# Kernel tuning notes

Hardware: AMD Instinct MI355X
Metric: run time of the kernel (lower is better)

The kernel has to match this reference:

```python
import jax, jax.numpy as jnp
import numpy as np

H, W = 480, 640  # config['loader']['resolution']
N = H * W
EPS = 1e-9


def _grid_indices():
    # matches torch.meshgrid(arange(H), arange(W)) stacked as (y, x): [1, N, 2]
    my, mx = jnp.meshgrid(jnp.arange(H, dtype=jnp.float32),
                          jnp.arange(W, dtype=jnp.float32), indexing='ij')
    return jnp.stack([my, mx], axis=-1).reshape(1, N, 2)


def setup_inputs() -> dict:
    key = jax.random.key(0)
    k1, k2 = jax.random.split(key)
    B, P = 8, 4
    return {
        'flow_maps_x': jax.random.normal(k1, (B, P, H, W), jnp.float32),
        'flow_maps_y': jax.random.normal(k2, (B, P, H, W), jnp.float32),
        'i': 0,
        'tref': 4,
    }


def reference(flow_maps_x, flow_maps_y, i, tref):
    B = flow_maps_x.shape[0]
    indices = _grid_indices()  # [1, N, 2] (y, x)

    # get_event_flow at the integer pixel grid == flattening the i-th flow map
    fy = flow_maps_y[:, i].reshape(B, N)
    fx = flow_maps_x[:, i].reshape(B, N)
    indices_flow = jnp.stack([fy, fx], axis=-1)  # [B, N, 2] (flow_y, flow_x)

    # event_propagation: warp grid to tref
    dt = jnp.asarray(tref - i, dtype=flow_maps_x.dtype)
    warped = indices + dt * indices_flow  # [B, N, 2]

    # purge_unfeasible: zero out mask for points leaving the image
    inside = ((warped[..., 0] >= 0) & (warped[..., 0] <= H - 1) &
              (warped[..., 1] >= 0) & (warped[..., 1] <= W - 1))
    mask = inside.astype(warped.dtype)[..., None]  # [B, N, 1]

    # get_interpolation: 4 bilinear neighbors, weights = prod of axis weights
    top_y = jnp.floor(warped[..., 0:1]); bot_y = top_y + 1.0
    left_x = jnp.floor(warped[..., 1:2]); right_x = left_x + 1.0
    idx = jnp.concatenate([
        jnp.concatenate([top_y, left_x], -1),
        jnp.concatenate([top_y, right_x], -1),
        jnp.concatenate([bot_y, left_x], -1),
        jnp.concatenate([bot_y, right_x], -1)], axis=1)  # [B, 4N, 2]
    ev4 = jnp.tile(warped, (1, 4, 1))
    w = jnp.clip(1.0 - jnp.abs(ev4 - idx), 0.0, 1.0)
    weights = w[..., 0:1] * w[..., 1:2]  # [B, 4N, 1]

    mask4 = jnp.tile(mask, (1, 4, 1))
    flow4 = jnp.tile(indices_flow, (1, 4, 1))
    flat = (idx[..., 0] * W + idx[..., 1]).astype(jnp.int32)  # [B, 4N]
    batch_ix = jnp.arange(B)[:, None]

    def splat(vals):  # vals [B, 4N, 1] -> [B, 1, H, W] scatter-add
        v = (vals * mask4)[..., 0]
        img = jnp.zeros((B, N), vals.dtype).at[batch_ix, flat].add(v, mode='drop')
        return img.reshape(B, 1, H, W)

    warped_weights = splat(weights)
    warped_flow_y = splat(weights * flow4[..., 0:1]) / (warped_weights + EPS)
    warped_flow_x = splat(weights * flow4[..., 1:2]) / (warped_weights + EPS)
    return warped_flow_x, warped_flow_y
```

## Files before the change

### kernel.cpp

```cpp
#include <hip/hip_runtime.h>
#include <stdint.h>

#define HH 480
#define WW 640
#define NN (HH * WW)
#define BB 8
#define PP 4
#define EPS 1e-9f

#define TW 64
#define TH 32
#define HALO 12
#define RGW (TW + 2 * HALO)
#define RGH (TH + 2 * HALO)
#define RGN (RGW * RGH)
#define NBX (WW / TW)
#define NBY (HH / TH)
#define NBLOCKS (NBX * NBY * BB)

#define BINSX (TW + 1)
#define BINSY (TH + 1)
#define NBINS (BINSX * BINSY)
#define CAP 4

#define SAFE_ID ((HALO << 7) | HALO)

#define SEGCAP 1024

__device__ __forceinline__ void gatomic(float* p, float v) {
    unsafeAtomicAdd(p, v);
}

__global__ __launch_bounds__(256)
void interleave_flow(const float* __restrict__ fx_all,
                     const float* __restrict__ fy_all,
                     const int* __restrict__ i_ptr,
                     float2* __restrict__ fxy2) {
    int t = blockIdx.x * blockDim.x + threadIdx.x;
    const int Q = NN / 4;
    if (t >= BB * Q) return;
    int b = t / Q, q = t - b * Q;
    int i = *i_ptr;
    const float4* fyp = (const float4*)(fy_all + (size_t)(b * PP + i) * NN);
    const float4* fxp = (const float4*)(fx_all + (size_t)(b * PP + i) * NN);
    float4 y4 = fyp[q], x4 = fxp[q];
    float2* o = fxy2 + (size_t)b * NN + (size_t)q * 4;
    o[0] = make_float2(y4.x, x4.x);
    o[1] = make_float2(y4.y, x4.y);
    o[2] = make_float2(y4.z, x4.z);
    o[3] = make_float2(y4.w, x4.w);
}

__global__ __launch_bounds__(256, 4)
void bin_gather_splat(const float2* __restrict__ fxy2,
                      const int* __restrict__ i_ptr,
                      const int* __restrict__ tref_ptr,
                      float* __restrict__ Sw, float* __restrict__ Swy, float* __restrict__ Swx,
                      unsigned* __restrict__ segcnt, int4* __restrict__ llist,
                      float* __restrict__ out) {
    __shared__ unsigned cnt[NBINS];
    __shared__ ushort4  ids4[NBINS];
    __shared__ unsigned lseg;
    const int tid = threadIdx.x;
    for (int e = tid; e < NBINS; e += 256) cnt[e] = 0;
    if (tid == 0) lseg = 0;
    __syncthreads();

    const int bx = blockIdx.x, by = blockIdx.y, b = blockIdx.z;
    const int bid = (b * NBY + by) * NBX + bx;
    int4* __restrict__ lseg_base = llist + (size_t)bid * SEGCAP;
    const int tx0 = bx * TW, ty0 = by * TH;
    const float dt = (float)(*tref_ptr - *i_ptr);
    const float2* __restrict__ fp2 = fxy2 + (size_t)b * NN;
    const size_t BN = (size_t)BB * NN;

    for (int sp = tid; sp < RGN; sp += 256) {
        int sy = sp / RGW, sx = sp - sy * RGW;
        int gy = ty0 - HALO + sy, gx = tx0 - HALO + sx;
        if ((unsigned)gy >= (unsigned)HH || (unsigned)gx >= (unsigned)WW) continue;
        int p = gy * WW + gx;
        float2 f2 = fp2[p];
        float fy = f2.x, fx = f2.y;
        float wyf = (float)gy + dt * fy;
        float wxf = (float)gx + dt * fx;
        if (!(wyf >= 0.0f && wyf <= (float)(HH - 1) &&
              wxf >= 0.0f && wxf <= (float)(WW - 1))) continue;
        float tyf = floorf(wyf), lxf = floorf(wxf);
        int iy0 = (int)tyf, ix0 = (int)lxf;
        int br = iy0 - ty0, bc = ix0 - tx0;

        bool overflow = false;
        if (br >= -1 && br < TH && bc >= -1 && bc < TW) {
            int bin = (br + 1) * BINSX + (bc + 1);
            unsigned slot = atomicAdd(&cnt[bin], 1u);
            if (slot < CAP)
                ((unsigned short*)&ids4[bin])[slot] = (unsigned short)((sy << 7) | sx);
            else overflow = true;
        }
        bool interior = ((unsigned)(gx - tx0) < (unsigned)TW) &&
                        ((unsigned)(gy - ty0) < (unsigned)TH);
        if (overflow || interior) {
            float fry = wyf - tyf, frx = wxf - lxf;
            float wts[4] = {(1.0f - fry) * (1.0f - frx),
                            (1.0f - fry) * frx,
                            fry * (1.0f - frx),
                            fry * frx};
#pragma unroll
            for (int k = 0; k < 4; ++k) {
                int iy = iy0 + (k >> 1), ix = ix0 + (k & 1);
                if ((unsigned)iy >= (unsigned)HH || (unsigned)ix >= (unsigned)WW) continue;
                bool inT = ((unsigned)(iy - ty0) < (unsigned)TH) &&
                           ((unsigned)(ix - tx0) < (unsigned)TW);
                int tnx = (ix >> 6) << 6;
                int tny = (iy >> 5) << 5;
                int ddx = gx < tnx ? tnx - gx : (gx > tnx + (TW - 1) ? gx - tnx - (TW - 1) : 0);
                int ddy = gy < tny ? tny - gy : (gy > tny + (TH - 1) ? gy - tny - (TH - 1) : 0);
                bool far = (ddx > HALO) || (ddy > HALO);
                if ((interior && far) || (overflow && inT)) {
                    int fi = b * NN + iy * WW + ix;
                    float w = wts[k];
                    unsigned slot = atomicAdd(&lseg, 1u);
                    if (slot < SEGCAP)
                        lseg_base[slot] = make_int4(fi, __float_as_int(w),
                                                    __float_as_int(w * fy),
                                                    __float_as_int(w * fx));
                }
            }
        }
    }
    __syncthreads();
    if (tid == 0) segcnt[bid] = lseg > SEGCAP ? SEGCAP : lseg;

    {
        const int c  = tid & 63;
        const int r0 = (tid >> 6) * 8;
        const float cxf = (float)(tx0 + c);

#define LOAD_SLOT(dst, idraw, nn, T) {                                        \
        bool valid = (unsigned)(T) < (nn);                                    \
        int sid = valid ? (int)(idraw) : SAFE_ID;                             \
        int sy_ = sid >> 7, sx_ = sid & 127;                                  \
        int gy_ = ty0 - HALO + sy_, gx_ = tx0 - HALO + sx_;                   \
        float2 f2_ = fp2[gy_ * WW + gx_];                                     \
        float wyf_ = (float)gy_ + dt * f2_.x;                                 \
        float wxf_ = (float)gx_ + dt * f2_.y;                                 \
        dst.x = valid ? wyf_ : -1.0e6f;                                       \
        dst.y = valid ? wxf_ : -1.0e6f;                                       \
        dst.z = f2_.x; dst.w = f2_.y; }

#define LOAD_ROW(d0,d1,d2,d3,d4,d5,d6,d7, brow) {                             \
        int bin0_ = (brow) * BINSX + c;                                       \
        unsigned na_ = cnt[bin0_];     ushort4 sa_ = ids4[bin0_];             \
        unsigned nb_ = cnt[bin0_ + 1]; ushort4 sb_ = ids4[bin0_ + 1];         \
        LOAD_SLOT(d0, sa_.x, na_, 0); LOAD_SLOT(d1, sa_.y, na_, 1);           \
        LOAD_SLOT(d2, sa_.z, na_, 2); LOAD_SLOT(d3, sa_.w, na_, 3);           \
        LOAD_SLOT(d4, sb_.x, nb_, 0); LOAD_SLOT(d5, sb_.y, nb_, 1);           \
        LOAD_SLOT(d6, sb_.z, nb_, 2); LOAD_SLOT(d7, sb_.w, nb_, 3); }

#define EVAL_SLOT(S) {                                                        \
        float ay_ = fmaxf(1.0f - fabsf(S.x - cyf), 0.0f);                     \
        float ax_ = fmaxf(1.0f - fabsf(S.y - cxf), 0.0f);                     \
        float w_ = ay_ * ax_;                                                 \
        ws += w_; wys += w_ * S.z; wxs += w_ * S.w; }

        float4 a0,a1,a2,a3,a4,a5,a6,a7;
        float4 b0,b1,b2,b3,b4,b5,b6,b7;
        LOAD_ROW(a0,a1,a2,a3,a4,a5,a6,a7, r0);
#pragma unroll
        for (int rr = 0; rr < 8; ++rr) {
            int r = r0 + rr;
            LOAD_ROW(b0,b1,b2,b3,b4,b5,b6,b7, r + 1);
            float cyf = (float)(ty0 + r);
            float ws = 0.f, wys = 0.f, wxs = 0.f;
            EVAL_SLOT(a0); EVAL_SLOT(a1); EVAL_SLOT(a2); EVAL_SLOT(a3);
            EVAL_SLOT(a4); EVAL_SLOT(a5); EVAL_SLOT(a6); EVAL_SLOT(a7);
            EVAL_SLOT(b0); EVAL_SLOT(b1); EVAL_SLOT(b2); EVAL_SLOT(b3);
            EVAL_SLOT(b4); EVAL_SLOT(b5); EVAL_SLOT(b6); EVAL_SLOT(b7);
            size_t o = (size_t)b * NN + (size_t)(ty0 + r) * WW + (tx0 + c);
            Sw[o] = ws; Swy[o] = wys; Swx[o] = wxs;
            float d = ws + EPS;
            out[o]      = wxs / d;
            out[BN + o] = wys / d;
            a0 = b0; a1 = b1; a2 = b2; a3 = b3;
            a4 = b4; a5 = b5; a6 = b6; a7 = b7;
        }
#undef LOAD_SLOT
#undef LOAD_ROW
#undef EVAL_SLOT
    }
}

__global__ __launch_bounds__(256)
void fix_add(const unsigned* __restrict__ segcnt, const int4* __restrict__ llist,
             float* __restrict__ Sw, float* __restrict__ Swy, float* __restrict__ Swx) {
    unsigned e = blockIdx.x * blockDim.x + threadIdx.x;
    unsigned seg = e / SEGCAP, idx = e - seg * SEGCAP;
    if (seg >= NBLOCKS || idx >= segcnt[seg]) return;
    int4 v = llist[e];
    gatomic(&Sw[v.x],  __int_as_float(v.y));
    gatomic(&Swy[v.x], __int_as_float(v.z));
    gatomic(&Swx[v.x], __int_as_float(v.w));
}

__global__ __launch_bounds__(256)
void fix_write(const unsigned* __restrict__ segcnt, const int4* __restrict__ llist,
               const float* __restrict__ Sw, const float* __restrict__ Swy,
               const float* __restrict__ Swx, float* __restrict__ out) {
    unsigned e = blockIdx.x * blockDim.x + threadIdx.x;
    unsigned seg = e / SEGCAP, idx = e - seg * SEGCAP;
    if (seg >= NBLOCKS || idx >= segcnt[seg]) return;
    int fi = llist[e].x;
    float d = Sw[fi] + EPS;
    out[fi] = Swx[fi] / d;
    out[(size_t)BB * NN + fi] = Swy[fi] / d;
}


__global__ void splat_kernel(const float* __restrict__ fx_all,
                             const float* __restrict__ fy_all,
                             const int* __restrict__ i_ptr,
                             const int* __restrict__ tref_ptr,
                             float* __restrict__ sum_w,
                             float* __restrict__ sum_wy,
                             float* __restrict__ sum_wx) {
    int t = blockIdx.x * blockDim.x + threadIdx.x;
    if (t >= BB * NN) return;
    int b = t / NN;
    int p = t - b * NN;
    int i = *i_ptr;
    float dt = (float)(*tref_ptr - i);
    const float fx = fx_all[(size_t)(b * PP + i) * NN + p];
    const float fy = fy_all[(size_t)(b * PP + i) * NN + p];
    float gy = (float)(p / WW);
    float gx = (float)(p - (p / WW) * WW);
    float wy = gy + dt * fy;
    float wx = gx + dt * fx;
    bool inside = (wy >= 0.0f) && (wy <= (float)(HH - 1)) &&
                  (wx >= 0.0f) && (wx <= (float)(WW - 1));
    if (!inside) return;
    float ty = floorf(wy);
    float lx = floorf(wx);
    int base = b * NN;
#pragma unroll
    for (int k = 0; k < 4; ++k) {
        float ny = ty + (float)(k >> 1);
        float nx = lx + (float)(k & 1);
        int iy = (int)ny;
        int ix = (int)nx;
        if (iy < 0 || iy >= HH || ix < 0 || ix >= WW) continue;
        float wgt_y = fminf(fmaxf(1.0f - fabsf(wy - ny), 0.0f), 1.0f);
        float wgt_x = fminf(fmaxf(1.0f - fabsf(wx - nx), 0.0f), 1.0f);
        float w = wgt_y * wgt_x;
        int fi = base + iy * WW + ix;
        gatomic(&sum_w[fi],  w);
        gatomic(&sum_wy[fi], w * fy);
        gatomic(&sum_wx[fi], w * fx);
    }
}

__global__ void finalize_kernel(const float* __restrict__ sum_w,
                                const float* __restrict__ sum_wy,
                                const float* __restrict__ sum_wx,
                                float* __restrict__ out) {
    int t = blockIdx.x * blockDim.x + threadIdx.x;
    if (t >= BB * NN) return;
    float denom = sum_w[t] + EPS;
    out[t]                   = sum_wx[t] / denom;
    out[(size_t)BB * NN + t] = sum_wy[t] / denom;
}


extern "C" void kernel_launch(void* const* d_in, const int* in_sizes, int n_in,
                              void* d_out, int out_size, void* d_ws, size_t ws_size,
                              hipStream_t stream) {
    const float* fx_all = (const float*)d_in[0];
    const float* fy_all = (const float*)d_in[1];
    const int* i_ptr    = (const int*)d_in[2];
    const int* tref_ptr = (const int*)d_in[3];
    float* out = (float*)d_out;

    const size_t BN = (size_t)BB * NN;
    const size_t s_bytes = 3 * BN * sizeof(float);
    const size_t f_bytes = BN * sizeof(float2);
    const size_t l_bytes = (size_t)NBLOCKS * SEGCAP * sizeof(int4);
    const size_t need = s_bytes + f_bytes + l_bytes + NBLOCKS * sizeof(unsigned);
    if (ws_size >= need) {
        float* Sw  = (float*)d_ws;
        float* Swy = Sw  + BN;
        float* Swx = Swy + BN;
        float2* fxy2 = (float2*)((char*)d_ws + s_bytes);
        int4* llist = (int4*)((char*)fxy2 + f_bytes);
        unsigned* segcnt = (unsigned*)((char*)llist + l_bytes);

        int itotal = (int)(BN / 4);
        interleave_flow<<<(itotal + 255) / 256, 256, 0, stream>>>(
            fx_all, fy_all, i_ptr, fxy2);
        dim3 grid(NBX, NBY, BB);
        bin_gather_splat<<<grid, 256, 0, stream>>>(fxy2, i_ptr, tref_ptr,
                                                   Sw, Swy, Swx, segcnt, llist, out);
        int fgrid = (NBLOCKS * SEGCAP) / 256;
        fix_add<<<fgrid, 256, 0, stream>>>(segcnt, llist, Sw, Swy, Swx);
        fix_write<<<fgrid, 256, 0, stream>>>(segcnt, llist, Sw, Swy, Swx, out);
    } else {
        float* sum_w  = (float*)d_ws;
        float* sum_wy = sum_w + BN;
        float* sum_wx = sum_wy + BN;
        hipMemsetAsync(d_ws, 0, 3 * BN * sizeof(float), stream);
        int total = (int)BN;
        int block = 256;
        int grid1 = (total + block - 1) / block;
        splat_kernel<<<grid1, block, 0, stream>>>(fx_all, fy_all, i_ptr, tref_ptr,
                                                  sum_w, sum_wy, sum_wx);
        finalize_kernel<<<grid1, block, 0, stream>>>(sum_w, sum_wy, sum_wx, out);
    }
}
```

Measured before the change: 71.73 us.

## Widen tiles to 128 columns and gather two output pixels per thread

Doubles the tile width so each block covers 128x32 pixels with the same 256 threads, and each thread now produces two adjacent output columns. The shared middle bin column is loaded once and evaluated for both pixels, and results are stored as float2. This reduces halo overhead per tile and redundant bin/flow gathers. In exchange it raises register pressure (occupancy hint lowered to 3), enlarges shared memory and the per-block overflow list, and packs source ids with 8-bit x fields.

Measured after the change: 89.28 us. +24.5%, slower.

```diff
diff --git a/kernel.cpp b/kernel.cpp
--- a/kernel.cpp
+++ b/kernel.cpp
@@ -8,7 +8,7 @@
 #define PP 4
 #define EPS 1e-9f
 
-#define TW 64
+#define TW 128
 #define TH 32
 #define HALO 12
 #define RGW (TW + 2 * HALO)
@@ -23,9 +23,9 @@
 #define NBINS (BINSX * BINSY)
 #define CAP 4
 
-#define SAFE_ID ((HALO << 7) | HALO)
-
-#define SEGCAP 1024
+#define SAFE_ID ((HALO << 8) | HALO)
+
+#define SEGCAP 2048
 
 __device__ __forceinline__ void gatomic(float* p, float v) {
     unsafeAtomicAdd(p, v);
@@ -51,7 +51,7 @@
     o[3] = make_float2(y4.w, x4.w);
 }
 
-__global__ __launch_bounds__(256, 4)
+__global__ __launch_bounds__(256, 3)
 void bin_gather_splat(const float2* __restrict__ fxy2,
                       const int* __restrict__ i_ptr,
                       const int* __restrict__ tref_ptr,
@@ -94,7 +94,7 @@
             int bin = (br + 1) * BINSX + (bc + 1);
             unsigned slot = atomicAdd(&cnt[bin], 1u);
             if (slot < CAP)
-                ((unsigned short*)&ids4[bin])[slot] = (unsigned short)((sy << 7) | sx);
+                ((unsigned short*)&ids4[bin])[slot] = (unsigned short)((sy << 8) | sx);
             else overflow = true;
         }
         bool interior = ((unsigned)(gx - tx0) < (unsigned)TW) &&
@@ -111,7 +111,7 @@
                 if ((unsigned)iy >= (unsigned)HH || (unsigned)ix >= (unsigned)WW) continue;
                 bool inT = ((unsigned)(iy - ty0) < (unsigned)TH) &&
                            ((unsigned)(ix - tx0) < (unsigned)TW);
-                int tnx = (ix >> 6) << 6;
+                int tnx = (ix >> 7) << 7;
                 int tny = (iy >> 5) << 5;
                 int ddx = gx < tnx ? tnx - gx : (gx > tnx + (TW - 1) ? gx - tnx - (TW - 1) : 0);
                 int ddy = gy < tny ? tny - gy : (gy > tny + (TH - 1) ? gy - tny - (TH - 1) : 0);
@@ -132,61 +132,103 @@
     if (tid == 0) segcnt[bid] = lseg > SEGCAP ? SEGCAP : lseg;
 
     {
-        const int c  = tid & 63;
+        const int c0 = (tid & 63) * 2;
         const int r0 = (tid >> 6) * 8;
-        const float cxf = (float)(tx0 + c);
+        const float cxL = (float)(tx0 + c0);
+        const float cxR = cxL + 1.0f;
 
 #define LOAD_SLOT(dst, idraw, nn, T) {                                        \
         bool valid = (unsigned)(T) < (nn);                                    \
         int sid = valid ? (int)(idraw) : SAFE_ID;                             \
-        int sy_ = sid >> 7, sx_ = sid & 127;                                  \
+        int sy_ = sid >> 8, sx_ = sid & 255;                                  \
         int gy_ = ty0 - HALO + sy_, gx_ = tx0 - HALO + sx_;                   \
         float2 f2_ = fp2[gy_ * WW + gx_];                                     \
         float wyf_ = (float)gy_ + dt * f2_.x;                                 \
         float wxf_ = (float)gx_ + dt * f2_.y;                                 \
-        dst.x = valid ? wyf_ : -1.0e6f;                                       \
-        dst.y = valid ? wxf_ : -1.0e6f;                                       \
+        dst.x = valid ? wyf_ : -1.0e6f;       \
+        dst.y = wxf_;                                                         \
         dst.z = f2_.x; dst.w = f2_.y; }
 
-#define LOAD_ROW(d0,d1,d2,d3,d4,d5,d6,d7, brow) {                             \
-        int bin0_ = (brow) * BINSX + c;                                       \
-        unsigned na_ = cnt[bin0_];     ushort4 sa_ = ids4[bin0_];             \
-        unsigned nb_ = cnt[bin0_ + 1]; ushort4 sb_ = ids4[bin0_ + 1];         \
-        LOAD_SLOT(d0, sa_.x, na_, 0); LOAD_SLOT(d1, sa_.y, na_, 1);           \
-        LOAD_SLOT(d2, sa_.z, na_, 2); LOAD_SLOT(d3, sa_.w, na_, 3);           \
-        LOAD_SLOT(d4, sb_.x, nb_, 0); LOAD_SLOT(d5, sb_.y, nb_, 1);           \
-        LOAD_SLOT(d6, sb_.z, nb_, 2); LOAD_SLOT(d7, sb_.w, nb_, 3); }
-
-#define EVAL_SLOT(S) {                                                        \
+#define LOAD_ROW3(P0,P1,P2,P3, Q0,Q1,Q2,Q3, S0,S1,S2,S3, brow) {              \
+        int binb_ = (brow) * BINSX + c0;                                      \
+        unsigned n0_ = cnt[binb_];     ushort4 i0_ = ids4[binb_];             \
+        unsigned n1_ = cnt[binb_ + 1]; ushort4 i1_ = ids4[binb_ + 1];         \
+        unsigned n2_ = cnt[binb_ + 2]; ushort4 i2_ = ids4[binb_ + 2];         \
+        LOAD_SLOT(P0, i0_.x, n0_, 0); LOAD_SLOT(P1, i0_.y, n0_, 1);           \
+        LOAD_SLOT(P2, i0_.z, n0_, 2); LOAD_SLOT(P3, i0_.w, n0_, 3);           \
+        LOAD_SLOT(Q0, i1_.x, n1_, 0); LOAD_SLOT(Q1, i1_.y, n1_, 1);           \
+        LOAD_SLOT(Q2, i1_.z, n1_, 2); LOAD_SLOT(Q3, i1_.w, n1_, 3);           \
+        LOAD_SLOT(S0, i2_.x, n2_, 0); LOAD_SLOT(S1, i2_.y, n2_, 1);           \
+        LOAD_SLOT(S2, i2_.z, n2_, 2); LOAD_SLOT(S3, i2_.w, n2_, 3); }
+
+#define LOAD_ROW3_A(brow) LOAD_ROW3(Ap0,Ap1,Ap2,Ap3,Aq0,Aq1,Aq2,Aq3,As0,As1,As2,As3, brow)
+#define LOAD_ROW3_B(brow) LOAD_ROW3(Bp0,Bp1,Bp2,Bp3,Bq0,Bq1,Bq2,Bq3,Bs0,Bs1,Bs2,Bs3, brow)
+
+#define EVAL_L(S) {                                                           \
         float ay_ = fmaxf(1.0f - fabsf(S.x - cyf), 0.0f);                     \
-        float ax_ = fmaxf(1.0f - fabsf(S.y - cxf), 0.0f);                     \
+        float ax_ = fmaxf(1.0f - fabsf(S.y - cxL), 0.0f);                     \
         float w_ = ay_ * ax_;                                                 \
-        ws += w_; wys += w_ * S.z; wxs += w_ * S.w; }
-
-        float4 a0,a1,a2,a3,a4,a5,a6,a7;
-        float4 b0,b1,b2,b3,b4,b5,b6,b7;
-        LOAD_ROW(a0,a1,a2,a3,a4,a5,a6,a7, r0);
-#pragma unroll
-        for (int rr = 0; rr < 8; ++rr) {
-            int r = r0 + rr;
-            LOAD_ROW(b0,b1,b2,b3,b4,b5,b6,b7, r + 1);
-            float cyf = (float)(ty0 + r);
-            float ws = 0.f, wys = 0.f, wxs = 0.f;
-            EVAL_SLOT(a0); EVAL_SLOT(a1); EVAL_SLOT(a2); EVAL_SLOT(a3);
-            EVAL_SLOT(a4); EVAL_SLOT(a5); EVAL_SLOT(a6); EVAL_SLOT(a7);
-            EVAL_SLOT(b0); EVAL_SLOT(b1); EVAL_SLOT(b2); EVAL_SLOT(b3);
-            EVAL_SLOT(b4); EVAL_SLOT(b5); EVAL_SLOT(b6); EVAL_SLOT(b7);
-            size_t o = (size_t)b * NN + (size_t)(ty0 + r) * WW + (tx0 + c);
-            Sw[o] = ws; Swy[o] = wys; Swx[o] = wxs;
-            float d = ws + EPS;
-            out[o]      = wxs / d;
-            out[BN + o] = wys / d;
-            a0 = b0; a1 = b1; a2 = b2; a3 = b3;
-            a4 = b4; a5 = b5; a6 = b6; a7 = b7;
-        }
+        wsL += w_; wysL += w_ * S.z; wxsL += w_ * S.w; }
+
+#define EVAL_R(S) {                                                           \
+        float ay_ = fmaxf(1.0f - fabsf(S.x - cyf), 0.0f);                     \
+        float ax_ = fmaxf(1.0f - fabsf(S.y - cxR), 0.0f);                     \
+        float w_ = ay_ * ax_;                                                 \
+        wsR += w_; wysR += w_ * S.z; wxsR += w_ * S.w; }
+
+#define EVAL_B(S) {                                                           \
+        float ay_ = fmaxf(1.0f - fabsf(S.x - cyf), 0.0f);                     \
+        float axL_ = fmaxf(1.0f - fabsf(S.y - cxL), 0.0f);                    \
+        float axR_ = fmaxf(1.0f - fabsf(S.y - cxR), 0.0f);                    \
+        float wL_ = ay_ * axL_, wR_ = ay_ * axR_;                             \
+        wsL += wL_; wysL += wL_ * S.z; wxsL += wL_ * S.w;                     \
+        wsR += wR_; wysR += wR_ * S.z; wxsR += wR_ * S.w; }
+
+#define EVAL_ROW(XP0,XP1,XP2,XP3,XQ0,XQ1,XQ2,XQ3,XS0,XS1,XS2,XS3,             \
+                 YP0,YP1,YP2,YP3,YQ0,YQ1,YQ2,YQ3,YS0,YS1,YS2,YS3, rowr) {     \
+        float cyf = (float)(ty0 + (rowr));                                    \
+        float wsL=0.f,wysL=0.f,wxsL=0.f,wsR=0.f,wysR=0.f,wxsR=0.f;            \
+        EVAL_L(XP0); EVAL_L(XP1); EVAL_L(XP2); EVAL_L(XP3);                   \
+        EVAL_L(YP0); EVAL_L(YP1); EVAL_L(YP2); EVAL_L(YP3);                   \
+        EVAL_B(XQ0); EVAL_B(XQ1); EVAL_B(XQ2); EVAL_B(XQ3);                   \
+        EVAL_B(YQ0); EVAL_B(YQ1); EVAL_B(YQ2); EVAL_B(YQ3);                   \
+        EVAL_R(XS0); EVAL_R(XS1); EVAL_R(XS2); EVAL_R(XS3);                   \
+        EVAL_R(YS0); EVAL_R(YS1); EVAL_R(YS2); EVAL_R(YS3);                   \
+        size_t o = (size_t)b * NN + (size_t)(ty0 + (rowr)) * WW + (tx0 + c0); \
+        *(float2*)&Sw[o]  = make_float2(wsL, wsR);                            \
+        *(float2*)&Swy[o] = make_float2(wysL, wysR);                          \
+        *(float2*)&Swx[o] = make_float2(wxsL, wxsR);                          \
+        float dL = wsL + EPS, dR = wsR + EPS;                                 \
+        *(float2*)&out[o]      = make_float2(wxsL / dL, wxsR / dR);           \
+        *(float2*)&out[BN + o] = make_float2(wysL / dL, wysR / dR); }
+
+#define EVAL_ROW_AB(rowr) EVAL_ROW(Ap0,Ap1,Ap2,Ap3,Aq0,Aq1,Aq2,Aq3,As0,As1,As2,As3, \
+                                   Bp0,Bp1,Bp2,Bp3,Bq0,Bq1,Bq2,Bq3,Bs0,Bs1,Bs2,Bs3, rowr)
+#define EVAL_ROW_BA(rowr) EVAL_ROW(Bp0,Bp1,Bp2,Bp3,Bq0,Bq1,Bq2,Bq3,Bs0,Bs1,Bs2,Bs3, \
+                                   Ap0,Ap1,Ap2,Ap3,Aq0,Aq1,Aq2,Aq3,As0,As1,As2,As3, rowr)
+
+        float4 Ap0,Ap1,Ap2,Ap3,Aq0,Aq1,Aq2,Aq3,As0,As1,As2,As3;
+        float4 Bp0,Bp1,Bp2,Bp3,Bq0,Bq1,Bq2,Bq3,Bs0,Bs1,Bs2,Bs3;
+        LOAD_ROW3_A(r0);
+        LOAD_ROW3_B(r0 + 1);
+        EVAL_ROW_AB(r0 + 0);  LOAD_ROW3_A(r0 + 2);
+        EVAL_ROW_BA(r0 + 1);  LOAD_ROW3_B(r0 + 3);
+        EVAL_ROW_AB(r0 + 2);  LOAD_ROW3_A(r0 + 4);
+        EVAL_ROW_BA(r0 + 3);  LOAD_ROW3_B(r0 + 5);
+        EVAL_ROW_AB(r0 + 4);  LOAD_ROW3_A(r0 + 6);
+        EVAL_ROW_BA(r0 + 5);  LOAD_ROW3_B(r0 + 7);
+        EVAL_ROW_AB(r0 + 6);  LOAD_ROW3_A(r0 + 8);
+        EVAL_ROW_BA(r0 + 7);
 #undef LOAD_SLOT
-#undef LOAD_ROW
-#undef EVAL_SLOT
+#undef LOAD_ROW3
+#undef LOAD_ROW3_A
+#undef LOAD_ROW3_B
+#undef EVAL_L
+#undef EVAL_R
+#undef EVAL_B
+#undef EVAL_ROW
+#undef EVAL_ROW_AB
+#undef EVAL_ROW_BA
     }
 }
 
```
